# Kernel tuning notes

Hardware: AMD Instinct MI355X
Metric: run time of the kernel (lower is better)

Reference implementation:

```python
import jax, jax.numpy as jnp
import numpy as np

DIM = 1024
N_HEADS = 16
HEAD_DIM = DIM // N_HEADS
SCALE = HEAD_DIM ** -0.5


def setup_inputs() -> dict:
    key = jax.random.key(0)
    k1, k2, k3 = jax.random.split(key, 3)
    x = jax.random.normal(k1, (4, 2048, DIM), dtype=jnp.float32)
    w_qkv = jax.random.normal(k2, (DIM, 3 * DIM), dtype=jnp.float32) * (DIM ** -0.5)
    w_proj = jax.random.normal(k3, (DIM, DIM), dtype=jnp.float32) * (DIM ** -0.5)
    b_proj = jnp.zeros((DIM,), dtype=jnp.float32)
    return {"x": x, "w_qkv": w_qkv, "w_proj": w_proj, "b_proj": b_proj}


def reference(x, w_qkv, w_proj, b_proj):
    b, s, d = x.shape
    # qkv projection (no bias), split into q, k, v with per-head layout
    qkv = (x @ w_qkv).reshape(b, s, 3, N_HEADS, HEAD_DIM)
    q, k, v = jnp.moveaxis(qkv, 2, 0)  # each [b, s, h, hd]
    # scaled dot-product attention
    scores = jnp.einsum('bqhd,bkhd->bhqk', q, k) * SCALE
    attn = jax.nn.softmax(scores, axis=-1)
    out = jnp.einsum('bhqk,bkhd->bqhd', attn, v).reshape(b, s, d)
    # output projection (with bias)
    return out @ w_proj + b_proj
```

## Files before the change

kernel.cpp:

```cpp
#include <hip/hip_runtime.h>

#define DIM 1024
#define NHEADS 16
#define HD 64
#define SEQ 2048
#define BATCH 4
#define MROWS (BATCH * SEQ)
#define N3 (3 * DIM)
#define SCALE 0.125f
#define LOG2E 1.4426950408889634f
#define SM_C (SCALE * LOG2E)
#define SMAX 16.0f

typedef __attribute__((ext_vector_type(8))) __bf16 bf16x8;
typedef __attribute__((ext_vector_type(4))) __bf16 bf16x4;
typedef __attribute__((ext_vector_type(4))) float f32x4;

#define MFMA16(a, b, c) __builtin_amdgcn_mfma_f32_16x16x32_bf16((a), (b), (c), 0, 0, 0)

#define GLDS16(g, l)                                                        \
  __builtin_amdgcn_global_load_lds(                                         \
      (const __attribute__((address_space(1))) void*)(g),                   \
      (__attribute__((address_space(3))) void*)(l), 16, 0, 0)

__device__ __forceinline__ unsigned short f2bf(float f) {
  union { float f; unsigned u; } v;
  v.f = f;
  unsigned r = v.u + 0x7fffu + ((v.u >> 16) & 1u);
  return (unsigned short)(r >> 16);
}

__device__ __forceinline__ float exp2_hw(float x) {
  float r;
  asm("v_exp_f32 %0, %1" : "=v"(r) : "v"(x));
  return r;
}


__global__ void cast_x_kernel(const float* __restrict__ x,
                              unsigned short* __restrict__ xb, int n4) {
  int i = blockIdx.x * blockDim.x + threadIdx.x;
  if (i >= n4) return;
  float4 v = ((const float4*)x)[i];
  ushort4 o;
  o.x = f2bf(v.x); o.y = f2bf(v.y); o.z = f2bf(v.z); o.w = f2bf(v.w);
  ((ushort4*)xb)[i] = o;
}

__global__ void tcast_kernel(const float* __restrict__ in,
                             unsigned short* __restrict__ out, int K, int N) {
  __shared__ float tile[32][33];
  int t = threadIdx.x;
  int c = t & 31, r8 = t >> 5;
  int n0 = blockIdx.x * 32, k0 = blockIdx.y * 32;
#pragma unroll
  for (int i = 0; i < 4; ++i) {
    int kr = r8 + i * 8;
    tile[kr][c] = in[(size_t)(k0 + kr) * N + n0 + c];
  }
  __syncthreads();
#pragma unroll
  for (int i = 0; i < 4; ++i) {
    int nr = r8 + i * 8;
    out[(size_t)(n0 + nr) * K + k0 + c] = f2bf(tile[c][nr]);
  }
}


__global__ __launch_bounds__(256, 3)
void gemm_qkv_kernel(const unsigned short* __restrict__ A,
                     const unsigned short* __restrict__ Bt,
                     unsigned short* __restrict__ Qb,
                     unsigned short* __restrict__ Kb,
                     unsigned short* __restrict__ Vt) {
  __shared__ __align__(16) unsigned short As[128 * 64];
  __shared__ __align__(16) unsigned short Bs[128 * 64];
  int t = threadIdx.x;
  int w = t >> 6, l = t & 63;
  int lane16 = l & 15, lhi = l >> 4;
  int mbase = blockIdx.y * 128, nbase = blockIdx.x * 128;
  int wm = (w >> 1) * 64, wn = (w & 1) * 64;

  const int srow = t >> 3;
  const int sslot = (t & 7) ^ ((t >> 3) & 7);
  const unsigned short* Ag = A + (size_t)(mbase + srow) * 1024 + sslot * 8;
  const unsigned short* Bg = Bt + (size_t)(nbase + srow) * 1024 + sslot * 8;

  const int sl0 = ((lhi ^ (lane16 & 7)) << 4);
  const char* Ard = (const char*)As + (wm + lane16) * 128;
  const char* Brd = (const char*)Bs + (wn + lane16) * 128;

  f32x4 acc[4][4];
  f32x4 z4 = {0.f, 0.f, 0.f, 0.f};
#pragma unroll
  for (int i = 0; i < 4; ++i)
#pragma unroll
    for (int j = 0; j < 4; ++j) acc[i][j] = z4;

  for (int kt = 0; kt < 1024; kt += 64) {
#pragma unroll
    for (int i = 0; i < 4; ++i) {
      GLDS16(Ag + (size_t)(i * 32) * 1024 + kt, (char*)As + i * 4096 + w * 1024);
      GLDS16(Bg + (size_t)(i * 32) * 1024 + kt, (char*)Bs + i * 4096 + w * 1024);
    }
    __syncthreads();
#pragma unroll
    for (int kh = 0; kh < 2; ++kh) {
      const int so = sl0 ^ (kh << 6);
      bf16x8 af[4], bfr[4];
#pragma unroll
      for (int mi = 0; mi < 4; ++mi)
        af[mi] = *(const bf16x8*)(Ard + mi * 2048 + so);
#pragma unroll
      for (int ni = 0; ni < 4; ++ni)
        bfr[ni] = *(const bf16x8*)(Brd + ni * 2048 + so);
#pragma unroll
      for (int mi = 0; mi < 4; ++mi)
#pragma unroll
        for (int ni = 0; ni < 4; ++ni)
          acc[mi][ni] = MFMA16(af[mi], bfr[ni], acc[mi][ni]);
    }
    __syncthreads();
  }

#pragma unroll
  for (int mi = 0; mi < 4; ++mi) {
#pragma unroll
    for (int ni = 0; ni < 4; ++ni) {
#pragma unroll
      for (int r = 0; r < 4; ++r) {
        int grow = mbase + wm + mi * 16 + (lhi << 2) + r;
        int gcol = nbase + wn + ni * 16 + lane16;
        int b = grow >> 11, s = grow & 2047;
        unsigned short val = f2bf(acc[mi][ni][r]);
        if (gcol < 1024) {
          int h = gcol >> 6, d = gcol & 63;
          Qb[((size_t)(b * 16 + h) * 2048 + s) * 64 + d] = val;
        } else if (gcol < 2048) {
          int n2 = gcol - 1024;
          int h = n2 >> 6, d = n2 & 63;
          Kb[((size_t)(b * 16 + h) * 2048 + s) * 64 + d] = val;
        } else {
          int n2 = gcol - 2048;
          int h = n2 >> 6, d = n2 & 63;
          Vt[((size_t)(b * 16 + h) * 64 + d) * 2048 + s] = val;
        }
      }
    }
  }
}


__global__ __launch_bounds__(512, 4)
void attn_kernel(const unsigned short* __restrict__ Qb,
                 const unsigned short* __restrict__ Kb,
                 const unsigned short* __restrict__ Vt,
                 unsigned short* __restrict__ attn) {
  __shared__ __align__(16) unsigned short Ks[2][4096];
  __shared__ __align__(16) unsigned short Vs[2][4096];
  __shared__ __align__(16) unsigned short Ps[8][32][72];

  const int t = threadIdx.x, wv = t >> 6, l = t & 63;
  const int lane16 = l & 15, lhi = l >> 4;

  const int bid = blockIdx.x;
  const int nid = (bid & 7) * 64 + (bid >> 3);
  const int qg = nid & 7, h = (nid >> 3) & 15, b = nid >> 7;

  const unsigned short* Qp = Qb + (size_t)(b * NHEADS + h) * SEQ * HD;
  const unsigned short* Kp = Kb + (size_t)(b * NHEADS + h) * SEQ * HD;
  const unsigned short* Vp = Vt + (size_t)(b * NHEADS + h) * HD * SEQ;

  const int q0 = qg * 256 + wv * 32;

  bf16x8 qa[2][2];
#pragma unroll
  for (int mi = 0; mi < 2; ++mi)
#pragma unroll
    for (int kh = 0; kh < 2; ++kh)
      qa[mi][kh] = *(const bf16x8*)(Qp + (size_t)(q0 + mi * 16 + lane16) * HD +
                                    kh * 32 + lhi * 8);

  const int srow = t >> 3;
  const unsigned short* kg = Kp + srow * HD + (((t & 7) ^ ((t >> 5) & 7)) * 8);
  const unsigned short* vg =
      Vp + (size_t)srow * SEQ + (((t & 7) ^ ((t >> 3) & 7)) * 8);

  const int key = lane16 & 7;
  const int off0 = (lhi ^ key) << 4;
  const int off1 = off0 ^ 64;
  const char* krd = (const char*)&Ks[0][0] + lane16 * 512;
  const char* vrd = (const char*)&Vs[0][0] + lane16 * 128;
  unsigned short* pwr = &Ps[wv][0][lane16 * 4];
  const unsigned short* prd = &Ps[wv][lane16][lhi * 8];

  f32x4 z4 = {0.f, 0.f, 0.f, 0.f};
  f32x4 o[2][4];
  float lsum[2][4];
#pragma unroll
  for (int mi = 0; mi < 2; ++mi)
#pragma unroll
    for (int nd = 0; nd < 4; ++nd) o[mi][nd] = z4;
#pragma unroll
  for (int mi = 0; mi < 2; ++mi)
#pragma unroll
    for (int r = 0; r < 4; ++r) lsum[mi][r] = 0.f;

  GLDS16(kg, (char*)&Ks[0][0] + wv * 1024);
  GLDS16(vg, (char*)&Vs[0][0] + wv * 1024);
  __syncthreads();

  int cur = 0;
  for (int ti = 0; ti < SEQ / 64; ++ti) {
    if (ti < SEQ / 64 - 1) {
      const int kb = (ti + 1) * 64;
      GLDS16(kg + (size_t)kb * HD, (char*)&Ks[cur ^ 1][0] + wv * 1024);
      GLDS16(vg + kb, (char*)&Vs[cur ^ 1][0] + wv * 1024);
    }

    const char* kp = krd + cur * 8192;
    bf16x8 kf[4][2];
#pragma unroll
    for (int ni = 0; ni < 4; ++ni) {
      kf[ni][0] = *(const bf16x8*)(kp + ni * 128 + off0);
      kf[ni][1] = *(const bf16x8*)(kp + ni * 128 + off1);
    }
#pragma unroll
    for (int mi = 0; mi < 2; ++mi) {
      f32x4 s[4];
#pragma unroll
      for (int ni = 0; ni < 4; ++ni) {
        f32x4 a = MFMA16(qa[mi][0], kf[ni][0], z4);
        s[ni] = MFMA16(qa[mi][1], kf[ni][1], a);
      }
#pragma unroll
      for (int r = 0; r < 4; ++r) {
        float p0 = exp2_hw(__builtin_fmaf(s[0][r], SM_C, -SMAX));
        float p1 = exp2_hw(__builtin_fmaf(s[1][r], SM_C, -SMAX));
        float p2 = exp2_hw(__builtin_fmaf(s[2][r], SM_C, -SMAX));
        float p3 = exp2_hw(__builtin_fmaf(s[3][r], SM_C, -SMAX));
        lsum[mi][r] += (p0 + p1) + (p2 + p3);
        bf16x4 pk;
        pk[0] = (__bf16)p0; pk[1] = (__bf16)p1;
        pk[2] = (__bf16)p2; pk[3] = (__bf16)p3;
        *(bf16x4*)(pwr + (mi * 16 + (lhi << 2) + r) * 72) = pk;
      }
    }

    bf16x8 pa[2][2];
#pragma unroll
    for (int mi = 0; mi < 2; ++mi)
#pragma unroll
      for (int kvh = 0; kvh < 2; ++kvh)
        pa[mi][kvh] = *(const bf16x8*)(prd + mi * 16 * 72 + kvh * 32);
    const char* vp2 = vrd + cur * 8192;
#pragma unroll
    for (int nd = 0; nd < 4; ++nd) {
      bf16x8 v0 = *(const bf16x8*)(vp2 + nd * 2048 + off0);
      bf16x8 v1 = *(const bf16x8*)(vp2 + nd * 2048 + off1);
#pragma unroll
      for (int mi = 0; mi < 2; ++mi) {
        o[mi][nd] = MFMA16(pa[mi][0], v0, o[mi][nd]);
        o[mi][nd] = MFMA16(pa[mi][1], v1, o[mi][nd]);
      }
    }
    __syncthreads();
    cur ^= 1;
  }

#pragma unroll
  for (int mi = 0; mi < 2; ++mi)
#pragma unroll
    for (int r = 0; r < 4; ++r) {
      float ls = lsum[mi][r];
      ls += __shfl_xor(ls, 1);
      ls += __shfl_xor(ls, 2);
      ls += __shfl_xor(ls, 4);
      ls += __shfl_xor(ls, 8);
      lsum[mi][r] = 1.0f / ls;
    }
  size_t orow_base = (size_t)b * SEQ;
#pragma unroll
  for (int mi = 0; mi < 2; ++mi)
#pragma unroll
    for (int nd = 0; nd < 4; ++nd)
#pragma unroll
      for (int r = 0; r < 4; ++r) {
        int row = q0 + mi * 16 + (lhi << 2) + r;
        attn[(orow_base + row) * DIM + h * HD + nd * 16 + lane16] =
            f2bf(o[mi][nd][r] * lsum[mi][r]);
      }
}


__global__ __launch_bounds__(256, 3)
void gemm_proj_kernel(const unsigned short* __restrict__ A,
                      const unsigned short* __restrict__ Bt,
                      const float* __restrict__ bias,
                      float* __restrict__ out) {
  __shared__ __align__(16) unsigned short As[128 * 64];
  __shared__ __align__(16) unsigned short Bs[128 * 64];
  int t = threadIdx.x;
  int w = t >> 6, l = t & 63;
  int lane16 = l & 15, lhi = l >> 4;
  int mbase = blockIdx.y * 128, nbase = blockIdx.x * 128;
  int wm = (w >> 1) * 64, wn = (w & 1) * 64;

  const int srow = t >> 3;
  const int sslot = (t & 7) ^ ((t >> 3) & 7);
  const unsigned short* Ag = A + (size_t)(mbase + srow) * 1024 + sslot * 8;
  const unsigned short* Bg = Bt + (size_t)(nbase + srow) * 1024 + sslot * 8;

  const int sl0 = ((lhi ^ (lane16 & 7)) << 4);
  const char* Ard = (const char*)As + (wm + lane16) * 128;
  const char* Brd = (const char*)Bs + (wn + lane16) * 128;

  f32x4 acc[4][4];
  f32x4 z4 = {0.f, 0.f, 0.f, 0.f};
#pragma unroll
  for (int i = 0; i < 4; ++i)
#pragma unroll
    for (int j = 0; j < 4; ++j) acc[i][j] = z4;

  for (int kt = 0; kt < 1024; kt += 64) {
#pragma unroll
    for (int i = 0; i < 4; ++i) {
      GLDS16(Ag + (size_t)(i * 32) * 1024 + kt, (char*)As + i * 4096 + w * 1024);
      GLDS16(Bg + (size_t)(i * 32) * 1024 + kt, (char*)Bs + i * 4096 + w * 1024);
    }
    __syncthreads();
#pragma unroll
    for (int kh = 0; kh < 2; ++kh) {
      const int so = sl0 ^ (kh << 6);
      bf16x8 af[4], bfr[4];
#pragma unroll
      for (int mi = 0; mi < 4; ++mi)
        af[mi] = *(const bf16x8*)(Ard + mi * 2048 + so);
#pragma unroll
      for (int ni = 0; ni < 4; ++ni)
        bfr[ni] = *(const bf16x8*)(Brd + ni * 2048 + so);
#pragma unroll
      for (int mi = 0; mi < 4; ++mi)
#pragma unroll
        for (int ni = 0; ni < 4; ++ni)
          acc[mi][ni] = MFMA16(af[mi], bfr[ni], acc[mi][ni]);
    }
    __syncthreads();
  }

#pragma unroll
  for (int mi = 0; mi < 4; ++mi) {
#pragma unroll
    for (int ni = 0; ni < 4; ++ni) {
#pragma unroll
      for (int r = 0; r < 4; ++r) {
        int grow = mbase + wm + mi * 16 + (lhi << 2) + r;
        int gcol = nbase + wn + ni * 16 + lane16;
        out[(size_t)grow * 1024 + gcol] = acc[mi][ni][r] + bias[gcol];
      }
    }
  }
}


extern "C" void kernel_launch(void* const* d_in, const int* in_sizes, int n_in,
                              void* d_out, int out_size, void* d_ws,
                              size_t ws_size, hipStream_t stream) {
  const float* x = (const float*)d_in[0];
  const float* w_qkv = (const float*)d_in[1];
  const float* w_proj = (const float*)d_in[2];
  const float* b_proj = (const float*)d_in[3];
  float* out = (float*)d_out;
  char* ws = (char*)d_ws;

  unsigned short* xb = (unsigned short*)(ws);
  unsigned short* attnb = (unsigned short*)(ws);
  unsigned short* wqkvT = (unsigned short*)(ws + (16ull << 20));
  unsigned short* wprojT = (unsigned short*)(ws + (22ull << 20));
  unsigned short* Qb = (unsigned short*)(ws + (24ull << 20));
  unsigned short* Kb = (unsigned short*)(ws + (40ull << 20));
  unsigned short* Vt = (unsigned short*)(ws + (56ull << 20));

  int n4 = MROWS * DIM / 4;
  cast_x_kernel<<<n4 / 256, 256, 0, stream>>>(x, xb, n4);
  tcast_kernel<<<dim3(N3 / 32, DIM / 32), 256, 0, stream>>>(w_qkv, wqkvT, DIM, N3);
  tcast_kernel<<<dim3(DIM / 32, DIM / 32), 256, 0, stream>>>(w_proj, wprojT, DIM, DIM);
  gemm_qkv_kernel<<<dim3(N3 / 128, MROWS / 128), 256, 0, stream>>>(xb, wqkvT, Qb, Kb, Vt);
  attn_kernel<<<512, 512, 0, stream>>>(Qb, Kb, Vt, attnb);
  gemm_proj_kernel<<<dim3(DIM / 128, MROWS / 128), 256, 0, stream>>>(attnb, wprojT, b_proj, out);
}
```

Measured before the change: 206.9 us.

## Merge cast/transpose prep kernels into one launch and prioritize MFMA waves in attention

The three preprocessing launches (x cast to bf16, and the transposed casts of both weight matrices) are folded into a single prep kernel that branches on block index, so two kernel launches and their gaps disappear. The attention inner loop wraps its QK and PV MFMA sections in s_setprio(1)/s_setprio(0), so waves issuing matrix ops get scheduler priority over waves doing exp/softmax work. The proj GEMM shared arrays are renamed, which has no speed effect. Risks: the prep kernel's shared tile is now allocated for every block, including the pure cast blocks, and the priority hints may not help overlap.

Measured after the change: 206.5 us. No clear change (-0.2%).

```diff
diff --git a/kernel.cpp b/kernel.cpp
--- a/kernel.cpp
+++ b/kernel.cpp
@@ -37,22 +37,13 @@
 }
 
 
-__global__ void cast_x_kernel(const float* __restrict__ x,
-                              unsigned short* __restrict__ xb, int n4) {
-  int i = blockIdx.x * blockDim.x + threadIdx.x;
-  if (i >= n4) return;
-  float4 v = ((const float4*)x)[i];
-  ushort4 o;
-  o.x = f2bf(v.x); o.y = f2bf(v.y); o.z = f2bf(v.z); o.w = f2bf(v.w);
-  ((ushort4*)xb)[i] = o;
-}
-
-__global__ void tcast_kernel(const float* __restrict__ in,
-                             unsigned short* __restrict__ out, int K, int N) {
+__device__ __forceinline__ void tcast_tile(const float* __restrict__ in,
+                                           unsigned short* __restrict__ out,
+                                           int K, int N, int bx, int by,
+                                           int t) {
   __shared__ float tile[32][33];
-  int t = threadIdx.x;
   int c = t & 31, r8 = t >> 5;
-  int n0 = blockIdx.x * 32, k0 = blockIdx.y * 32;
+  int n0 = bx * 32, k0 = by * 32;
 #pragma unroll
   for (int i = 0; i < 4; ++i) {
     int kr = r8 + i * 8;
@@ -63,6 +54,28 @@
   for (int i = 0; i < 4; ++i) {
     int nr = r8 + i * 8;
     out[(size_t)(n0 + nr) * K + k0 + c] = f2bf(tile[c][nr]);
+  }
+}
+
+__global__ void prep_kernel(const float* __restrict__ x,
+                            unsigned short* __restrict__ xb,
+                            const float* __restrict__ wqkv,
+                            unsigned short* __restrict__ wqkvT,
+                            const float* __restrict__ wproj,
+                            unsigned short* __restrict__ wprojT) {
+  const int bid = blockIdx.x, t = threadIdx.x;
+  if (bid < 8192) {
+    int i = bid * 256 + t;
+    float4 v = ((const float4*)x)[i];
+    ushort4 o;
+    o.x = f2bf(v.x); o.y = f2bf(v.y); o.z = f2bf(v.z); o.w = f2bf(v.w);
+    ((ushort4*)xb)[i] = o;
+  } else if (bid < 11264) {
+    int local = bid - 8192;
+    tcast_tile(wqkv, wqkvT, DIM, N3, local % 96, local / 96, t);
+  } else {
+    int local = bid - 11264;
+    tcast_tile(wproj, wprojT, DIM, DIM, local % 32, local / 32, t);
   }
 }
 
@@ -228,11 +241,13 @@
 #pragma unroll
     for (int mi = 0; mi < 2; ++mi) {
       f32x4 s[4];
+      __builtin_amdgcn_s_setprio(1);
 #pragma unroll
       for (int ni = 0; ni < 4; ++ni) {
         f32x4 a = MFMA16(qa[mi][0], kf[ni][0], z4);
         s[ni] = MFMA16(qa[mi][1], kf[ni][1], a);
       }
+      __builtin_amdgcn_s_setprio(0);
 #pragma unroll
       for (int r = 0; r < 4; ++r) {
         float p0 = exp2_hw(__builtin_fmaf(s[0][r], SM_C, -SMAX));
@@ -254,6 +269,7 @@
       for (int kvh = 0; kvh < 2; ++kvh)
         pa[mi][kvh] = *(const bf16x8*)(prd + mi * 16 * 72 + kvh * 32);
     const char* vp2 = vrd + cur * 8192;
+    __builtin_amdgcn_s_setprio(1);
 #pragma unroll
     for (int nd = 0; nd < 4; ++nd) {
       bf16x8 v0 = *(const bf16x8*)(vp2 + nd * 2048 + off0);
@@ -264,6 +280,7 @@
         o[mi][nd] = MFMA16(pa[mi][1], v1, o[mi][nd]);
       }
     }
+    __builtin_amdgcn_s_setprio(0);
     __syncthreads();
     cur ^= 1;
   }
@@ -298,8 +315,8 @@
                       const unsigned short* __restrict__ Bt,
                       const float* __restrict__ bias,
                       float* __restrict__ out) {
-  __shared__ __align__(16) unsigned short As[128 * 64];
-  __shared__ __align__(16) unsigned short Bs[128 * 64];
+  __shared__ __align__(16) unsigned short Asp[128 * 64];
+  __shared__ __align__(16) unsigned short Bsp[128 * 64];
   int t = threadIdx.x;
   int w = t >> 6, l = t & 63;
   int lane16 = l & 15, lhi = l >> 4;
@@ -312,8 +329,8 @@
   const unsigned short* Bg = Bt + (size_t)(nbase + srow) * 1024 + sslot * 8;
 
   const int sl0 = ((lhi ^ (lane16 & 7)) << 4);
-  const char* Ard = (const char*)As + (wm + lane16) * 128;
-  const char* Brd = (const char*)Bs + (wn + lane16) * 128;
+  const char* Ard = (const char*)Asp + (wm + lane16) * 128;
+  const char* Brd = (const char*)Bsp + (wn + lane16) * 128;
 
   f32x4 acc[4][4];
   f32x4 z4 = {0.f, 0.f, 0.f, 0.f};
@@ -325,8 +342,8 @@
   for (int kt = 0; kt < 1024; kt += 64) {
 #pragma unroll
     for (int i = 0; i < 4; ++i) {
-      GLDS16(Ag + (size_t)(i * 32) * 1024 + kt, (char*)As + i * 4096 + w * 1024);
-      GLDS16(Bg + (size_t)(i * 32) * 1024 + kt, (char*)Bs + i * 4096 + w * 1024);
+      GLDS16(Ag + (size_t)(i * 32) * 1024 + kt, (char*)Asp + i * 4096 + w * 1024);
+      GLDS16(Bg + (size_t)(i * 32) * 1024 + kt, (char*)Bsp + i * 4096 + w * 1024);
     }
     __syncthreads();
 #pragma unroll
@@ -381,10 +398,7 @@
   unsigned short* Kb = (unsigned short*)(ws + (40ull << 20));
   unsigned short* Vt = (unsigned short*)(ws + (56ull << 20));
 
-  int n4 = MROWS * DIM / 4;
-  cast_x_kernel<<<n4 / 256, 256, 0, stream>>>(x, xb, n4);
-  tcast_kernel<<<dim3(N3 / 32, DIM / 32), 256, 0, stream>>>(w_qkv, wqkvT, DIM, N3);
-  tcast_kernel<<<dim3(DIM / 32, DIM / 32), 256, 0, stream>>>(w_proj, wprojT, DIM, DIM);
+  prep_kernel<<<12288, 256, 0, stream>>>(x, xb, w_qkv, wqkvT, w_proj, wprojT);
   gemm_qkv_kernel<<<dim3(N3 / 128, MROWS / 128), 256, 0, stream>>>(xb, wqkvT, Qb, Kb, Vt);
   attn_kernel<<<512, 512, 0, stream>>>(Qb, Kb, Vt, attnb);
   gemm_proj_kernel<<<dim3(DIM / 128, MROWS / 128), 256, 0, stream>>>(attnb, wprojT, b_proj, out);
```
